# Kernel optimization log

Hardware: AMD Instinct MI355X
Metric: run time of the kernel (lower is better)

Reference implementation:

```python
import jax, jax.numpy as jnp
import numpy as np

EPS = 1e-5
NEG_SLOPE = 0.2


def _minmax(a):
    m = jnp.min(a)
    return (a - m) / (jnp.max(a) - m)


def _bn(x2d, gamma, beta):
    # train-mode BatchNorm1d: stats over axis 0 (biased variance)
    mu = x2d.mean(0)
    var = x2d.var(0)
    return gamma * (x2d - mu) * jax.lax.rsqrt(var + EPS) + beta


def _leaky(a):
    return jnp.where(a >= 0, a, NEG_SLOPE * a)


def setup_inputs() -> dict:
    key = jax.random.key(0)
    ks = jax.random.split(key, 10)
    B, C, N = 256, 1024, 80
    stdv = 1.0 / np.sqrt(C)
    return {
        "x": jax.random.normal(ks[0], (B, C, N), jnp.float32),
        "out1": jax.random.normal(ks[1], (B, N), jnp.float32),
        "adj_param": jax.random.uniform(ks[2], (N, N), jnp.float32),
        "static_weight": jax.random.uniform(ks[3], (C, C), jnp.float32, -stdv, stdv),
        "dynamic_weight": jax.random.uniform(ks[4], (C, C), jnp.float32, -stdv, stdv),
        "conv_global_w": jax.random.normal(ks[5], (C, C), jnp.float32) * 0.02,
        "conv_global_b": jnp.zeros((C,), jnp.float32),
        "conv_co_w": jax.random.normal(ks[6], (N, 2 * C), jnp.float32) * 0.02,
        "conv_co_b": jnp.zeros((N,), jnp.float32),
        "bn_gamma": jnp.ones((C,), jnp.float32),
        "bn_beta": jnp.zeros((C,), jnp.float32),
        "bng_gamma": jnp.ones((C,), jnp.float32),
        "bng_beta": jnp.zeros((C,), jnp.float32),
    }


def reference(x, out1, adj_param, static_weight, dynamic_weight,
              conv_global_w, conv_global_b, conv_co_w, conv_co_b,
              bn_gamma, bn_beta, bng_gamma, bng_beta):
    B, C, N = x.shape

    # ---- static GCN ----
    sadj = _minmax(adj_param)                               # (N,N)
    D = jax.lax.rsqrt(sadj.sum(1))                          # A.sum(1)^-0.5
    adj = D[:, None] * sadj.T * D[None, :]                  # gen_adj, diag matmuls as broadcast
    support = jnp.einsum('bcn,co->bno', x, static_weight)   # (B,N,C)
    h = jnp.einsum('nm,bmo->bno', adj, support)             # (B,N,C)
    h = _bn(h.reshape(-1, C), bn_gamma, bn_beta).reshape(B, N, C)
    out_static = _leaky(h).transpose(0, 2, 1)               # (B,C,N)
    x2 = x + out_static

    # ---- dynamic graph construction ----
    glb = x2.mean(2)                                        # GAP over nodes -> (B,C)
    glb = glb @ conv_global_w.T + conv_global_b             # 1x1 conv
    glb = _leaky(_bn(glb, bng_gamma, bng_beta))             # BN over batch (L=1)
    cat = jnp.concatenate([jnp.broadcast_to(glb[:, :, None], (B, C, N)), x2], axis=1)  # (B,2C,N)
    dadj = jnp.einsum('oc,bcn->bon', conv_co_w, cat) + conv_co_b[None, :, None]        # (B,N,N)
    dadj = _minmax(dadj)

    # ---- adjacency loss ----
    t1 = jnp.einsum('bn,bnm->bm', out1, dadj) / N
    loss = jnp.sum(jnp.linalg.norm(out1 - t1, axis=1))
    loss = loss + jnp.sum(jnp.linalg.norm((dadj - sadj).reshape(B, -1), axis=1))

    # ---- dynamic GCN ----
    Dd = jax.lax.rsqrt(dadj.sum(2))                         # (B,N)
    tadj = Dd[:, :, None] * dadj.transpose(0, 2, 1) * Dd[:, None, :]
    sup = jnp.einsum('bcn,co->bno', x2, dynamic_weight)
    h2 = jnp.einsum('bnm,bmo->bno', tadj, sup)
    h2 = _bn(h2.reshape(-1, C), bn_gamma, bn_beta).reshape(B, N, C).transpose(0, 2, 1)
    h2 = _leaky(h2)                                         # (B,C,N)
    return h2, loss
```

## Files before the change

### kernel.cpp

```cpp
#include <hip/hip_runtime.h>
#include <hip/hip_bf16.h>
#include <math.h>

#define TPB 256

constexpr int   B_  = 256;
constexpr int   C_  = 1024;
constexpr int   N_  = 80;
constexpr int   BNr = B_ * N_;
constexpr int   CN  = C_ * N_;
constexpr long  BCN = (long)B_ * C_ * N_;
constexpr int   NN  = N_ * N_;
constexpr int   BNN = B_ * NN;
constexpr float EPSf = 1e-5f;

typedef __bf16 bf16x8 __attribute__((ext_vector_type(8)));
typedef float  f32x4  __attribute__((ext_vector_type(4)));

__device__ __forceinline__ float leakyf(float v) { return v >= 0.0f ? v : 0.2f * v; }

__device__ __forceinline__ ushort f2bf(float f) {
  __hip_bfloat16 h = __float2bfloat16(f);
  ushort u; __builtin_memcpy(&u, &h, 2); return u;
}
__device__ __forceinline__ float b2f(ushort u) {
  __hip_bfloat16 h; __builtin_memcpy(&h, &u, 2);
  return __bfloat162float(h);
}

#define GLOBAL_AS __attribute__((address_space(1)))
#define LDS_AS    __attribute__((address_space(3)))
__device__ __forceinline__ void load_lds16(const void* g, void* l) {
  __builtin_amdgcn_global_load_lds((const GLOBAL_AS void*)g, (LDS_AS void*)l, 16, 0, 0);
}

__global__ __launch_bounds__(256) void k_prep_all(
    const float* __restrict__ Ws, const float* __restrict__ Wd,
    const float* __restrict__ Wco, const float* __restrict__ Wg,
    ushort* __restrict__ Wts, ushort* __restrict__ Wtd,
    ushort* __restrict__ Wco1t, ushort* __restrict__ Wco2t, ushort* __restrict__ Wg_bf,
    float* __restrict__ zbase,
    const float* __restrict__ ap, float* __restrict__ sadj,
    ushort* __restrict__ adj_bf, float* __restrict__ lossa) {
  __shared__ float sh[NN];
  __shared__ float red[TPB];
  __shared__ float sD[N_];
  __shared__ float s_lo, s_hi;
  const int t = threadIdx.x;
  const int blk = blockIdx.x;
  if (blk < 2048) {
    const float* W = (blk < 1024) ? Ws : Wd;
    ushort* Wt = (blk < 1024) ? Wts : Wtd;
    const int bb = blk & 1023;
    const int bx = bb & 31, by = bb >> 5;
    const int tx = t % 32, ty = t / 32;
    const int r0 = by * 32, c0 = bx * 32;
#pragma unroll
    for (int k = 0; k < 4; ++k) sh[(ty + 8 * k) * 33 + tx] = W[(size_t)(r0 + ty + 8 * k) * C_ + c0 + tx];
    __syncthreads();
#pragma unroll
    for (int k = 0; k < 4; ++k) Wt[(size_t)(c0 + ty + 8 * k) * C_ + r0 + tx] = f2bf(sh[tx * 33 + ty + 8 * k]);
  } else if (blk < 2208) {
    const int i4 = ((blk - 2048) * TPB + t) * 4;
    const int o = i4 >> 11, k = i4 & 2047;
    float4 v = *(const float4*)&Wco[(size_t)o * 2048 + k];
    ushort4 u;
    u.x = f2bf(v.x); u.y = f2bf(v.y); u.z = f2bf(v.z); u.w = f2bf(v.w);
    if (k < C_) *(ushort4*)&Wco1t[(size_t)o * C_ + k] = u;
    else        *(ushort4*)&Wco2t[(size_t)o * C_ + (k - C_)] = u;
  } else if (blk < 3232) {
    const long i4 = ((long)(blk - 2208) * TPB + t) * 4;
    float4 v = *(const float4*)&Wg[i4];
    ushort4 u;
    u.x = f2bf(v.x); u.y = f2bf(v.y); u.z = f2bf(v.z); u.w = f2bf(v.w);
    *(ushort4*)&Wg_bf[i4] = u;
  } else if (blk < 3258) {
    const int i = ((blk - 3232) * TPB + t) * 4;
    float4 z = make_float4(0.f, 0.f, 0.f, 0.f);
    *(float4*)&zbase[i] = z;
  } else {
    float lo = 3.4e38f, hi = -3.4e38f;
    for (int i = t; i < NN; i += TPB) { float v = ap[i]; sh[i] = v; lo = fminf(lo, v); hi = fmaxf(hi, v); }
    red[t] = lo; __syncthreads();
    for (int o = 128; o > 0; o >>= 1) { if (t < o) red[t] = fminf(red[t], red[t + o]); __syncthreads(); }
    if (t == 0) s_lo = red[0];
    __syncthreads();
    red[t] = hi; __syncthreads();
    for (int o = 128; o > 0; o >>= 1) { if (t < o) red[t] = fmaxf(red[t], red[t + o]); __syncthreads(); }
    if (t == 0) s_hi = red[0];
    __syncthreads();
    const float inv = 1.0f / (s_hi - s_lo);
    for (int i = t; i < NN; i += TPB) { float v = (sh[i] - s_lo) * inv; sh[i] = v; sadj[i] = v; }
    __syncthreads();
    if (t < N_) { float sum = 0.f; for (int m = 0; m < N_; ++m) sum += sh[t * N_ + m]; sD[t] = rsqrtf(sum); }
    if (t == 0) *lossa = 0.0f;
    __syncthreads();
    for (int i = t; i < N_ * 96; i += TPB) {
      const int n = i / 96, m = i % 96;
      adj_bf[i] = f2bf((m < N_) ? sD[n] * sh[m * N_ + n] * sD[m] : 0.0f);
    }
  }
}

__global__ __launch_bounds__(256) void k_fold_mfma(const float* __restrict__ Xf32,
                                                   const ushort* __restrict__ Xbf,
                                                   const void* __restrict__ adjsrc,
                                                   ushort* __restrict__ outp, int mode,
                                                   const float* __restrict__ bmin,
                                                   const float* __restrict__ bmax,
                                                   const float* __restrict__ sadj,
                                                   const float* __restrict__ out1,
                                                   float* __restrict__ lossa) {
  __shared__ __align__(16) ushort sX[128][104];
  __shared__ __align__(16) ushort sAdj[80][104];
  __shared__ float sD[N_];
  __shared__ float rl[TPB], rh[TPB];
  __shared__ float s_lo, s_inv;
  const int t = threadIdx.x;
  const int b  = blockIdx.x >> 3;
  const int c0 = (blockIdx.x & 7) * 128;

  if (mode == 0) {
    const ushort* ab = (const ushort*)adjsrc;
    for (int i = t; i < (N_ * 96) / 4; i += TPB) {
      ushort4 v = *(const ushort4*)&ab[i * 4];
      *(ushort4*)&sAdj[(i * 4) / 96][(i * 4) % 96] = v;
    }
    __syncthreads();
  } else {
    rl[t] = (t < 160) ? bmin[t] : 3.4e38f;
    rh[t] = (t < 160) ? bmax[t] : -3.4e38f;
    __syncthreads();
    for (int o = 128; o > 0; o >>= 1) {
      if (t < o) { rl[t] = fminf(rl[t], rl[t + o]); rh[t] = fmaxf(rh[t], rh[t + o]); }
      __syncthreads();
    }
    if (t == 0) { s_lo = rl[0]; s_inv = 1.0f / (rh[0] - rl[0]); }
    __syncthreads();
    const float lo = s_lo, inv = s_inv;
    float* sF = (float*)&sX[0][0];
    const float* db = (const float*)adjsrc + (size_t)b * NN;
    for (int i = t; i < NN / 4; i += TPB) {
      float4 v = *(const float4*)&db[i * 4];
      v.x = (v.x - lo) * inv; v.y = (v.y - lo) * inv;
      v.z = (v.z - lo) * inv; v.w = (v.w - lo) * inv;
      *(float4*)&sF[i * 4] = v;
    }
    __syncthreads();
    if (t < N_) { float s = 0.f; for (int m = 0; m < N_; ++m) s += sF[t * N_ + m]; sD[t] = rsqrtf(s); }
    __syncthreads();
    for (int i = t; i < N_ * 96; i += TPB) {
      const int n = i / 96, m = i % 96;
      sAdj[n][m] = f2bf((m < N_) ? sF[m * N_ + n] * sD[n] * sD[m] : 0.0f);
    }
    __syncthreads();
    if ((blockIdx.x & 7) == 0) {
      const float* o1 = out1 + b * N_;
      float p2 = 0.f;
      for (int i = t; i < NN; i += TPB) { const float d = sF[i] - sadj[i]; p2 += d * d; }
      float p1 = 0.f;
      if (t < N_) {
        float a = 0.f;
        for (int n = 0; n < N_; ++n) a += o1[n] * sF[n * N_ + t];
        const float d = o1[t] - a * (1.0f / N_);
        p1 = d * d;
      }
      rl[t] = p2; rh[t] = p1;
      __syncthreads();
      for (int o = 128; o > 0; o >>= 1) {
        if (t < o) { rl[t] += rl[t + o]; rh[t] += rh[t + o]; }
        __syncthreads();
      }
      if (t == 0) atomicAdd(lossa, sqrtf(rl[0]) + sqrtf(rh[0]));
      __syncthreads();
    }
  }

  if (mode == 0) {
    const float* Xb = Xf32 + ((size_t)b * C_ + c0) * N_;
    for (int i = t; i < (128 * N_) / 4; i += TPB) {
      float4 v = *(const float4*)&Xb[i * 4];
      const int r = (i * 4) / N_, m = (i * 4) % N_;
      ushort4 u; u.x = f2bf(v.x); u.y = f2bf(v.y); u.z = f2bf(v.z); u.w = f2bf(v.w);
      *(ushort4*)&sX[r][m] = u;
    }
  } else {
    const ushort* Xb = Xbf + ((size_t)b * C_ + c0) * N_;
    for (int i = t; i < (128 * N_) / 8; i += TPB) {
      const int r = i / 10, m = (i % 10) * 8;
      uint4 v = *(const uint4*)&Xb[(size_t)r * N_ + m];
      *(uint4*)&sX[r][m] = v;
    }
  }
  for (int i = t; i < (128 * 16) / 4; i += TPB) {
    const int r = i / 4, m = 80 + (i % 4) * 4;
    ushort4 z; z.x = 0; z.y = 0; z.z = 0; z.w = 0;
    *(ushort4*)&sX[r][m] = z;
  }
  __syncthreads();

  const int lane = t & 63, wid = t >> 6;
  const int l16 = lane & 15, lq = lane >> 4;
  f32x4 acc[2][5];
#pragma unroll
  for (int i = 0; i < 2; ++i)
#pragma unroll
    for (int j = 0; j < 5; ++j) { f32x4 z = {0.f, 0.f, 0.f, 0.f}; acc[i][j] = z; }
  bf16x8 af[2][3], bfr[5][3];
#pragma unroll
  for (int i = 0; i < 2; ++i)
#pragma unroll
    for (int kk = 0; kk < 3; ++kk)
      af[i][kk] = *(const bf16x8*)&sX[wid * 32 + i * 16 + l16][kk * 32 + lq * 8];
#pragma unroll
  for (int j = 0; j < 5; ++j)
#pragma unroll
    for (int kk = 0; kk < 3; ++kk)
      bfr[j][kk] = *(const bf16x8*)&sAdj[j * 16 + l16][kk * 32 + lq * 8];
#pragma unroll
  for (int i = 0; i < 2; ++i)
#pragma unroll
    for (int j = 0; j < 5; ++j)
#pragma unroll
      for (int kk = 0; kk < 3; ++kk)
        acc[i][j] = __builtin_amdgcn_mfma_f32_16x16x32_bf16(af[i][kk], bfr[j][kk], acc[i][j], 0, 0, 0);

  ushort* ob = outp + (size_t)b * CN;
#pragma unroll
  for (int i = 0; i < 2; ++i) {
    const int c = c0 + wid * 32 + i * 16 + lq * 4;
#pragma unroll
    for (int j = 0; j < 5; ++j) {
      const int n = j * 16 + l16;
      ushort4 u;
      u.x = f2bf(acc[i][j][0]); u.y = f2bf(acc[i][j][1]);
      u.z = f2bf(acc[i][j][2]); u.w = f2bf(acc[i][j][3]);
      *(ushort4*)&ob[(size_t)n * C_ + c] = u;
    }
  }
}

__global__ __launch_bounds__(256, 2) void k_gemm_160(const ushort* __restrict__ A,
                                                     const ushort* __restrict__ Bt,
                                                     void* __restrict__ outp, int out_bf,
                                                     float* __restrict__ bnsum,
                                                     float* __restrict__ bnsq) {
  __shared__ ushort sA[2][160 * 64];
  __shared__ ushort sB[2][128 * 64];
  const int t = threadIdx.x;
  const int lane = t & 63, wid = t >> 6;
  const int wm = wid >> 1, wn = wid & 1;
  const int l16 = lane & 15, lq = lane >> 4;

  const int lin = blockIdx.x;
  const int xcd = lin & 7, bi = lin >> 3;
  const int tm = xcd * 16 + (bi >> 3);
  const int tn = bi & 7;
  const int m0 = tm * 160, o0 = tn * 128;

  const int srow = t >> 3;
  const int sswz = ((t & 7) ^ ((t >> 3) & 7)) * 8;

  f32x4 acc[5][4];
#pragma unroll
  for (int i = 0; i < 5; ++i)
#pragma unroll
    for (int j = 0; j < 4; ++j) { f32x4 z = {0.f, 0.f, 0.f, 0.f}; acc[i][j] = z; }

#define STA(PAR, ROWB, KT) load_lds16(A  + (size_t)(m0 + (ROWB) + srow) * C_ + (KT) * 64 + sswz, \
                                      &sA[PAR][((ROWB) + (wid << 3)) * 64])
#define STB(PAR, ROWB, KT) load_lds16(Bt + (size_t)(o0 + (ROWB) + srow) * C_ + (KT) * 64 + sswz, \
                                      &sB[PAR][((ROWB) + (wid << 3)) * 64])
#define STAGE_T(PAR, KT) { STA(PAR, 0, KT); STA(PAR, 32, KT); STA(PAR, 64, KT); \
                           STA(PAR, 96, KT); STA(PAR, 128, KT); \
                           STB(PAR, 0, KT); STB(PAR, 32, KT); STB(PAR, 64, KT); STB(PAR, 96, KT); }

#define PH(PAR, KK, STAGES, VMW)                                                          \
  {                                                                                       \
    STAGES                                                                                \
    bf16x8 afr[5], bfr[4];                                                                \
    _Pragma("unroll") for (int fi = 0; fi < 5; ++fi)                                      \
      afr[fi] = *(const bf16x8*)&sA[PAR][(wm * 80 + fi * 16 + l16) * 64 +                 \
                                         (((KK) * 4 + lq) ^ (l16 & 7)) * 8];              \
    _Pragma("unroll") for (int gi = 0; gi < 4; ++gi)                                      \
      bfr[gi] = *(const bf16x8*)&sB[PAR][(wn * 64 + gi * 16 + l16) * 64 +                 \
                                         (((KK) * 4 + lq) ^ (l16 & 7)) * 8];              \
    asm volatile("s_barrier" ::: "memory");                                               \
    asm volatile("s_waitcnt lgkmcnt(0)" ::: "memory");                                    \
    __builtin_amdgcn_s_setprio(1);                                                        \
    _Pragma("unroll") for (int fi = 0; fi < 5; ++fi)                                      \
      _Pragma("unroll") for (int gi = 0; gi < 4; ++gi)                                    \
        acc[fi][gi] = __builtin_amdgcn_mfma_f32_16x16x32_bf16(afr[fi], bfr[gi],           \
                                                              acc[fi][gi], 0, 0, 0);      \
    __builtin_amdgcn_s_setprio(0);                                                        \
    VMW                                                                                   \
    asm volatile("s_barrier" ::: "memory");                                               \
  }

  STAGE_T(0, 0);
  asm volatile("s_waitcnt vmcnt(0)" ::: "memory");
  asm volatile("s_barrier" ::: "memory");

  for (int i = 0; i < 8; ++i) {
    const int t1 = 2 * i + 1, t2 = 2 * i + 2;
    PH(0, 0, { STAGE_T(1, t1); }, {})
    PH(0, 1, {}, { asm volatile("s_waitcnt vmcnt(0)" ::: "memory"); })
    PH(1, 0, { if (i < 7) STAGE_T(0, t2); }, {})
    PH(1, 1, {}, { if (i < 7) { asm volatile("s_waitcnt vmcnt(0)" ::: "memory"); } })
  }

#pragma unroll
  for (int fi = 0; fi < 5; ++fi) {
    const int mg = m0 + wm * 80 + fi * 16 + lq * 4;
    const int b  = mg / 80;
    const int n0 = mg - b * 80;
#pragma unroll
    for (int gi = 0; gi < 4; ++gi) {
      const int og = o0 + wn * 64 + gi * 16 + l16;
      const size_t off = (size_t)b * CN + (size_t)og * N_ + n0;
      if (out_bf) {
        ushort4 u;
        u.x = f2bf(acc[fi][gi][0]); u.y = f2bf(acc[fi][gi][1]);
        u.z = f2bf(acc[fi][gi][2]); u.w = f2bf(acc[fi][gi][3]);
        *(ushort4*)((ushort*)outp + off) = u;
      } else {
        *(f32x4*)((float*)outp + off) = acc[fi][gi];
      }
    }
  }

  {
    float* redS = (float*)&sA[0][0];
    float* redQ = redS + 1024;
    const int slot = wm * 4 + lq;
#pragma unroll
    for (int gi = 0; gi < 4; ++gi) {
      float s = 0.f, q = 0.f;
#pragma unroll
      for (int fi = 0; fi < 5; ++fi)
#pragma unroll
        for (int r = 0; r < 4; ++r) { const float v = acc[fi][gi][r]; s += v; q += v * v; }
      const int ol = wn * 64 + gi * 16 + l16;
      redS[ol * 8 + slot] = s;
      redQ[ol * 8 + slot] = q;
    }
    __syncthreads();
    if (t < 128) {
      float s = 0.f, q = 0.f;
#pragma unroll
      for (int k = 0; k < 8; ++k) { s += redS[t * 8 + k]; q += redQ[t * 8 + k]; }
      atomicAdd(&bnsum[o0 + t], s);
      atomicAdd(&bnsq[o0 + t], q);
    }
  }
#undef STA
#undef STB
#undef STAGE_T
#undef PH
}

__global__ __launch_bounds__(256) void k_dadj_mfma(const ushort* __restrict__ A,
                                                   const ushort* __restrict__ Bw,
                                                   const float* __restrict__ go,
                                                   const float* __restrict__ bco,
                                                   float* __restrict__ dadj,
                                                   float* __restrict__ bmin,
                                                   float* __restrict__ bmax) {
  __shared__ ushort smA[128 * 32];
  __shared__ ushort smB[80 * 32];
  const int t = threadIdx.x;
  const int lane = t & 63, wid = t >> 6;
  const int m0 = blockIdx.x * 128;
  const int rto = t >> 2, ch = t & 3;
  const size_t gA0 = (size_t)(m0 + rto) * C_ + (size_t)ch * 8;
  ushort* ldsA = smA + wid * 512;
  const int l16 = lane & 15, lq = lane >> 4;
  const int wrow = wid * 32;
  f32x4 zero = {0.f, 0.f, 0.f, 0.f};
  f32x4 acc[2][5];
#pragma unroll
  for (int i = 0; i < 2; ++i)
#pragma unroll
    for (int j = 0; j < 5; ++j) acc[i][j] = zero;
  for (int k0 = 0; k0 < C_; k0 += 32) {
    load_lds16(A + gA0 + k0,            ldsA);
    load_lds16(A + gA0 + 64 * C_ + k0,  ldsA + 2048);
    {
      const int idx = t;
      uint4 v = *(const uint4*)&Bw[(size_t)(idx >> 2) * C_ + k0 + (idx & 3) * 8];
      *(uint4*)&smB[idx * 8] = v;
      if (t < 64) {
        const int idx2 = 256 + t;
        uint4 v2 = *(const uint4*)&Bw[(size_t)(idx2 >> 2) * C_ + k0 + (idx2 & 3) * 8];
        *(uint4*)&smB[idx2 * 8] = v2;
      }
    }
    __syncthreads();
    bf16x8 af[2], bfr[5];
#pragma unroll
    for (int i = 0; i < 2; ++i) af[i]  = *(const bf16x8*)&smA[(wrow + i * 16 + l16) * 32 + lq * 8];
#pragma unroll
    for (int j = 0; j < 5; ++j) bfr[j] = *(const bf16x8*)&smB[(j * 16 + l16) * 32 + lq * 8];
#pragma unroll
    for (int i = 0; i < 2; ++i)
#pragma unroll
      for (int j = 0; j < 5; ++j)
        acc[i][j] = __builtin_amdgcn_mfma_f32_16x16x32_bf16(af[i], bfr[j], acc[i][j], 0, 0, 0);
    __syncthreads();
  }
  float vlo = 3.4e38f, vhi = -3.4e38f;
#pragma unroll
  for (int i = 0; i < 2; ++i) {
    const int mg = m0 + wrow + i * 16 + lq * 4;
    const int b  = mg / 80;
    const int n0 = mg - b * 80;
    const float* gob = go + b * N_;
#pragma unroll
    for (int j = 0; j < 5; ++j) {
      const int o = j * 16 + l16;
      const float g = gob[o] + bco[o];
      f32x4 v = acc[i][j];
      v[0] += g; v[1] += g; v[2] += g; v[3] += g;
      vlo = fminf(vlo, fminf(fminf(v[0], v[1]), fminf(v[2], v[3])));
      vhi = fmaxf(vhi, fmaxf(fmaxf(v[0], v[1]), fmaxf(v[2], v[3])));
      *(f32x4*)&dadj[(size_t)b * NN + (size_t)o * N_ + n0] = v;
    }
  }
  float* red = (float*)smA;
  red[t] = vlo; red[TPB + t] = vhi;
  __syncthreads();
  for (int o = 128; o > 0; o >>= 1) {
    if (t < o) {
      red[t] = fminf(red[t], red[t + o]);
      red[TPB + t] = fmaxf(red[TPB + t], red[TPB + t + o]);
    }
    __syncthreads();
  }
  if (t == 0) { bmin[blockIdx.x] = red[0]; bmax[blockIdx.x] = red[TPB]; }
}

__global__ __launch_bounds__(256) void k_glb_mfma(const ushort* __restrict__ A,
                                                  const ushort* __restrict__ Bw,
                                                  const float* __restrict__ bias,
                                                  float* __restrict__ outp,
                                                  float* __restrict__ gsum,
                                                  float* __restrict__ gsq) {
  __shared__ ushort smA[2][64 * 32];
  __shared__ ushort smB[2][64 * 32];
  const int t = threadIdx.x;
  const int lane = t & 63, wid = t >> 6;
  const int o0 = blockIdx.x * 64, m0 = blockIdx.y * 64;
  const int rto = t >> 2, ch = t & 3;
  const size_t gA0 = (size_t)(m0 + rto) * C_ + (size_t)ch * 8;
  const size_t gB0 = (size_t)(o0 + rto) * C_ + (size_t)ch * 8;
  const int l16 = lane & 15, lq = lane >> 4;
  const int wm = wid & 1, wn = wid >> 1;
  f32x4 zero = {0.f, 0.f, 0.f, 0.f};
  f32x4 acc[2][2];
#pragma unroll
  for (int i = 0; i < 2; ++i)
#pragma unroll
    for (int j = 0; j < 2; ++j) acc[i][j] = zero;
  for (int k0 = 0; k0 < C_; k0 += 64) {
    load_lds16(A  + gA0 + k0,       smA[0] + wid * 512);
    load_lds16(A  + gA0 + k0 + 32,  smA[1] + wid * 512);
    load_lds16(Bw + gB0 + k0,       smB[0] + wid * 512);
    load_lds16(Bw + gB0 + k0 + 32,  smB[1] + wid * 512);
    __syncthreads();
#pragma unroll
    for (int h = 0; h < 2; ++h) {
      bf16x8 af[2], bfr[2];
#pragma unroll
      for (int i = 0; i < 2; ++i) af[i]  = *(const bf16x8*)&smA[h][(wm * 32 + i * 16 + l16) * 32 + lq * 8];
#pragma unroll
      for (int j = 0; j < 2; ++j) bfr[j] = *(const bf16x8*)&smB[h][(wn * 32 + j * 16 + l16) * 32 + lq * 8];
#pragma unroll
      for (int i = 0; i < 2; ++i)
#pragma unroll
        for (int j = 0; j < 2; ++j)
          acc[i][j] = __builtin_amdgcn_mfma_f32_16x16x32_bf16(af[i], bfr[j], acc[i][j], 0, 0, 0);
    }
    __syncthreads();
  }
  float ssv[2] = {0.f, 0.f}, sqv[2] = {0.f, 0.f};
#pragma unroll
  for (int i = 0; i < 2; ++i) {
    const int mg = m0 + wm * 32 + i * 16 + lq * 4;
#pragma unroll
    for (int j = 0; j < 2; ++j) {
      const int og = o0 + wn * 32 + j * 16 + l16;
      const float bs = bias[og];
      f32x4 v = acc[i][j];
#pragma unroll
      for (int r = 0; r < 4; ++r) {
        const float val = v[r] + bs;
        outp[(size_t)(mg + r) * C_ + og] = val;
        ssv[j] += val; sqv[j] += val * val;
      }
    }
  }
  {
    float* redS = (float*)&smA[0][0];
    float* redQ = redS + 512;
    const int slot = wm * 4 + lq;
#pragma unroll
    for (int j = 0; j < 2; ++j) {
      const int ol = wn * 32 + j * 16 + l16;
      redS[ol * 8 + slot] = ssv[j];
      redQ[ol * 8 + slot] = sqv[j];
    }
    __syncthreads();
    if (t < 64) {
      float s = 0.f, q = 0.f;
#pragma unroll
      for (int k = 0; k < 8; ++k) { s += redS[t * 8 + k]; q += redQ[t * 8 + k]; }
      atomicAdd(&gsum[o0 + t], s);
      atomicAdd(&gsq[o0 + t], q);
    }
  }
}

__global__ __launch_bounds__(256) void k_go_mfma(const float* __restrict__ glb1,
                                                 const ushort* __restrict__ Bw,
                                                 const float* __restrict__ gsum,
                                                 const float* __restrict__ gsq,
                                                 const float* __restrict__ gg,
                                                 const float* __restrict__ gb,
                                                 float* __restrict__ go) {
  __shared__ ushort smA[128 * 32];
  __shared__ ushort smB[80 * 32];
  __shared__ float pgm[C_], pmu[C_], pgb[C_];
  const int t = threadIdx.x;
  const int lane = t & 63, wid = t >> 6;
  const int kbase = blockIdx.x * 128;
  const int m0 = blockIdx.y * 128;
  const int rto = t >> 2, ch = t & 3;
  const int l16 = lane & 15, lq = lane >> 4;
  const int wrow = wid * 32;
  for (int c = t; c < C_; c += TPB) {
    const float mu = gsum[c] * (1.0f / B_);
    const float var = gsq[c] * (1.0f / B_) - mu * mu;
    pgm[c] = gg[c] * rsqrtf(var + EPSf); pmu[c] = mu; pgb[c] = gb[c];
  }
  __syncthreads();
  f32x4 zero = {0.f, 0.f, 0.f, 0.f};
  f32x4 acc[2][5];
#pragma unroll
  for (int i = 0; i < 2; ++i)
#pragma unroll
    for (int j = 0; j < 5; ++j) acc[i][j] = zero;
  for (int kk0 = 0; kk0 < 128; kk0 += 32) {
    const int k0 = kbase + kk0;
#pragma unroll
    for (int h = 0; h < 2; ++h) {
      const float* src = &glb1[(size_t)(m0 + h * 64 + rto) * C_ + k0 + ch * 8];
      float4 a0 = *(const float4*)src;
      float4 a1 = *(const float4*)(src + 4);
      float av[8] = {a0.x, a0.y, a0.z, a0.w, a1.x, a1.y, a1.z, a1.w};
      ushort4 u0, u1;
      const int cb = k0 + ch * 8;
      u0.x = f2bf(leakyf(pgm[cb+0]*(av[0]-pmu[cb+0])+pgb[cb+0]));
      u0.y = f2bf(leakyf(pgm[cb+1]*(av[1]-pmu[cb+1])+pgb[cb+1]));
      u0.z = f2bf(leakyf(pgm[cb+2]*(av[2]-pmu[cb+2])+pgb[cb+2]));
      u0.w = f2bf(leakyf(pgm[cb+3]*(av[3]-pmu[cb+3])+pgb[cb+3]));
      u1.x = f2bf(leakyf(pgm[cb+4]*(av[4]-pmu[cb+4])+pgb[cb+4]));
      u1.y = f2bf(leakyf(pgm[cb+5]*(av[5]-pmu[cb+5])+pgb[cb+5]));
      u1.z = f2bf(leakyf(pgm[cb+6]*(av[6]-pmu[cb+6])+pgb[cb+6]));
      u1.w = f2bf(leakyf(pgm[cb+7]*(av[7]-pmu[cb+7])+pgb[cb+7]));
      *(ushort4*)&smA[h * 2048 + t * 8]     = u0;
      *(ushort4*)&smA[h * 2048 + t * 8 + 4] = u1;
    }
    {
      const int idx = t;
      uint4 v = *(const uint4*)&Bw[(size_t)(idx >> 2) * C_ + k0 + (idx & 3) * 8];
      *(uint4*)&smB[idx * 8] = v;
      if (t < 64) {
        const int idx2 = 256 + t;
        uint4 v2 = *(const uint4*)&Bw[(size_t)(idx2 >> 2) * C_ + k0 + (idx2 & 3) * 8];
        *(uint4*)&smB[idx2 * 8] = v2;
      }
    }
    __syncthreads();
    bf16x8 af[2], bfr[5];
#pragma unroll
    for (int i = 0; i < 2; ++i) af[i]  = *(const bf16x8*)&smA[(wrow + i * 16 + l16) * 32 + lq * 8];
#pragma unroll
    for (int j = 0; j < 5; ++j) bfr[j] = *(const bf16x8*)&smB[(j * 16 + l16) * 32 + lq * 8];
#pragma unroll
    for (int i = 0; i < 2; ++i)
#pragma unroll
      for (int j = 0; j < 5; ++j)
        acc[i][j] = __builtin_amdgcn_mfma_f32_16x16x32_bf16(af[i], bfr[j], acc[i][j], 0, 0, 0);
    __syncthreads();
  }
#pragma unroll
  for (int i = 0; i < 2; ++i) {
    const int mg = m0 + wrow + i * 16 + lq * 4;
#pragma unroll
    for (int j = 0; j < 5; ++j) {
      const int o = j * 16 + l16;
#pragma unroll
      for (int r = 0; r < 4; ++r)
        atomicAdd(&go[(size_t)(mg + r) * N_ + o], acc[i][j][r]);
    }
  }
}

__global__ __launch_bounds__(256) void k_x2_fused(
    const float* __restrict__ x, ushort* __restrict__ hx,
    const float* __restrict__ g, const float* __restrict__ be,
    const float* __restrict__ ssum, const float* __restrict__ ssq,
    ushort* __restrict__ x2t, ushort* __restrict__ glb0b) {
  __shared__ float s[64][85];
  __shared__ float pg[64], pm[64], pb[64];
  const int t = threadIdx.x;
  const long row0 = (long)blockIdx.x * 64;
  const int b = (int)(row0 >> 10), c0 = (int)(row0 & 1023);
  if (t < 64) {
    const int c = c0 + t;
    const float mu = ssum[c] * (1.0f / BNr);
    const float var = ssq[c] * (1.0f / BNr) - mu * mu;
    const float rstd = rsqrtf(var + EPSf);
    pg[t] = g[c] * rstd; pm[t] = mu; pb[t] = be[c];
  }
  __syncthreads();
  const float* xb = x  + row0 * N_;
  ushort*      hb = hx + row0 * N_;
  for (int i4 = t; i4 < (64 * N_) / 4; i4 += TPB) {
    const int e = i4 * 4, r = e / N_, n = e % N_;
    float4 xv = *(const float4*)&xb[e];
    ushort4 hu = *(const ushort4*)&hb[e];
    const float gm = pg[r], m = pm[r], bb = pb[r];
    float4 o;
    o.x = xv.x + leakyf(gm * (b2f(hu.x) - m) + bb);
    o.y = xv.y + leakyf(gm * (b2f(hu.y) - m) + bb);
    o.z = xv.z + leakyf(gm * (b2f(hu.z) - m) + bb);
    o.w = xv.w + leakyf(gm * (b2f(hu.w) - m) + bb);
    *(float4*)&s[r][n] = o;
    ushort4 ou;
    ou.x = f2bf(o.x); ou.y = f2bf(o.y); ou.z = f2bf(o.z); ou.w = f2bf(o.w);
    *(ushort4*)&hb[e] = ou;
  }
  __syncthreads();
  const int tx = t % 16, ty = t / 16;
  ushort* tb = x2t + (size_t)b * CN + c0 + tx * 4;
#pragma unroll
  for (int u = 0; u < 5; ++u) {
    const int n = ty + 16 * u;
    ushort4 v;
    v.x = f2bf(s[tx * 4 + 0][n]); v.y = f2bf(s[tx * 4 + 1][n]);
    v.z = f2bf(s[tx * 4 + 2][n]); v.w = f2bf(s[tx * 4 + 3][n]);
    *(ushort4*)&tb[(size_t)n * C_] = v;
  }
  {
    const int r = t >> 2, q = t & 3;
    float sacc = 0.f;
    for (int n = q; n < N_; n += 4) sacc += s[r][n];
    sacc += __shfl_down(sacc, 1);
    sacc += __shfl_down(sacc, 2);
    if (q == 0) glb0b[(size_t)b * C_ + c0 + r] = f2bf(sacc * (1.0f / N_));
  }
}

__global__ void k_final(const ushort* __restrict__ h2, float* __restrict__ outp,
                        const float* __restrict__ g, const float* __restrict__ be,
                        const float* __restrict__ ssum, const float* __restrict__ ssq,
                        const float* __restrict__ lossa) {
  const long i = ((long)blockIdx.x * TPB + threadIdx.x) * 4;
  const int c = (int)((i / N_) % C_);
  ushort4 hu = *(const ushort4*)&h2[i];
  const float mu = ssum[c] * (1.0f / BNr);
  const float rstd = rsqrtf(ssq[c] * (1.0f / BNr) - mu * mu + EPSf);
  const float gm = g[c] * rstd, bb = be[c];
  float4 v;
  v.x = leakyf(gm * (b2f(hu.x) - mu) + bb);
  v.y = leakyf(gm * (b2f(hu.y) - mu) + bb);
  v.z = leakyf(gm * (b2f(hu.z) - mu) + bb);
  v.w = leakyf(gm * (b2f(hu.w) - mu) + bb);
  *(float4*)&outp[i] = v;
  if (blockIdx.x == 0 && threadIdx.x == 0) outp[BCN] = *lossa;
}

extern "C" void kernel_launch(void* const* d_in, const int* in_sizes, int n_in,
                              void* d_out, int out_size, void* d_ws, size_t ws_size,
                              hipStream_t stream) {
  const float* x    = (const float*)d_in[0];
  const float* out1 = (const float*)d_in[1];
  const float* ap   = (const float*)d_in[2];
  const float* Ws   = (const float*)d_in[3];
  const float* Wd   = (const float*)d_in[4];
  const float* Wg   = (const float*)d_in[5];
  const float* bg   = (const float*)d_in[6];
  const float* Wco  = (const float*)d_in[7];
  const float* bco  = (const float*)d_in[8];
  const float* bn_g  = (const float*)d_in[9];
  const float* bn_b  = (const float*)d_in[10];
  const float* bng_g = (const float*)d_in[11];
  const float* bng_b = (const float*)d_in[12];
  float* out = (float*)d_out;

  float* w = (float*)d_ws;
  float* sadj  = w;
  float* dadj  = sadj + NN;
  float* glb0  = dadj + BNN;
  float* glb1  = glb0 + B_ * C_;
  float* go    = glb1 + B_ * C_;
  float* ssum1 = go + BNr;
  float* ssq1  = ssum1 + C_;
  float* ssum2 = ssq1 + C_;
  float* ssq2  = ssum2 + C_;
  float* gsum  = ssq2 + C_;
  float* gsq   = gsum + C_;
  float* bmin  = gsq + C_;
  float* bmax  = bmin + 512;
  float* lossa = bmax + 512;
  ushort* ub   = (ushort*)(((uintptr_t)(lossa + 1) + 255) & ~(uintptr_t)255);
  ushort* xa_bf  = ub;
  ushort* hT_bf  = xa_bf + BCN;
  ushort* Wts    = hT_bf + BCN;
  ushort* Wtd    = Wts + (size_t)C_ * C_;
  ushort* Wco2t  = Wtd + (size_t)C_ * C_;
  ushort* adj_bf = Wco2t + (size_t)N_ * C_;
  ushort* Wg_bf   = (ushort*)dadj;
  ushort* Wco1t   = (ushort*)dadj + (size_t)C_ * C_;
  ushort* glb0_bf = (ushort*)glb0;
  ushort* x2t_bf  = xa_bf;

  k_prep_all<<<3259, TPB, 0, stream>>>(Ws, Wd, Wco, Wg, Wts, Wtd, Wco1t, Wco2t, Wg_bf,
                                       go, ap, sadj, adj_bf, lossa);

  k_fold_mfma<<<B_ * 8, TPB, 0, stream>>>(x, hT_bf, adj_bf, xa_bf, 0, bmin, bmax,
                                          sadj, out1, lossa);
  k_gemm_160<<<1024, TPB, 0, stream>>>(xa_bf, Wts, hT_bf, 1, ssum1, ssq1);
  k_x2_fused<<<(B_ * C_) / 64, TPB, 0, stream>>>(x, hT_bf, bn_g, bn_b, ssum1, ssq1,
                                                 x2t_bf, glb0_bf);

  k_glb_mfma<<<dim3(C_ / 64, B_ / 64), TPB, 0, stream>>>(glb0_bf, Wg_bf, bg, glb1, gsum, gsq);
  k_go_mfma<<<dim3(8, B_ / 128), TPB, 0, stream>>>(glb1, Wco1t, gsum, gsq, bng_g, bng_b, go);
  k_dadj_mfma<<<BNr / 128, TPB, 0, stream>>>(x2t_bf, Wco2t, go, bco, dadj, bmin, bmax);

  k_fold_mfma<<<B_ * 8, TPB, 0, stream>>>(x, hT_bf, dadj, xa_bf, 1, bmin, bmax,
                                          sadj, out1, lossa);
  k_gemm_160<<<1024, TPB, 0, stream>>>(xa_bf, Wtd, hT_bf, 1, ssum2, ssq2);
  k_final<<<(int)(BCN / (4 * TPB)), TPB, 0, stream>>>(hT_bf, out, bn_g, bn_b, ssum2, ssq2, lossa);
}
```

Before: 467.2 us.

## Build dynamic normalized adjacency once per batch in a separate kernel

The per-batch normalized dynamic adjacency and loss terms move out of the fold kernel into a new k_tadj kernel that runs one block per batch. Before, each of the 8 blocks per batch recomputed the same min/max reduction, degree normalization and bf16 transpose. The fold kernel now reads the precomputed bf16 adjacency and the X rows straight from global memory into MFMA fragments, skipping LDS staging and barriers. In exchange it adds a kernel launch and a global round trip for the adjacency. Fragments are read from global without LDS reuse, which may cost more memory traffic.

Measured after the change: 443.9 us. 5.0% less time.

```diff
diff --git a/kernel.cpp b/kernel.cpp
--- a/kernel.cpp
+++ b/kernel.cpp
@@ -12,6 +12,7 @@
 constexpr long  BCN = (long)B_ * C_ * N_;
 constexpr int   NN  = N_ * N_;
 constexpr int   BNN = B_ * NN;
+constexpr int   ADJP = N_ * 96;
 constexpr float EPSf = 1e-5f;
 
 typedef __bf16 bf16x8 __attribute__((ext_vector_type(8)));
@@ -95,135 +96,118 @@
     if (t < N_) { float sum = 0.f; for (int m = 0; m < N_; ++m) sum += sh[t * N_ + m]; sD[t] = rsqrtf(sum); }
     if (t == 0) *lossa = 0.0f;
     __syncthreads();
-    for (int i = t; i < N_ * 96; i += TPB) {
+    for (int i = t; i < ADJP; i += TPB) {
       const int n = i / 96, m = i % 96;
       adj_bf[i] = f2bf((m < N_) ? sD[n] * sh[m * N_ + n] * sD[m] : 0.0f);
     }
   }
 }
 
-__global__ __launch_bounds__(256) void k_fold_mfma(const float* __restrict__ Xf32,
-                                                   const ushort* __restrict__ Xbf,
-                                                   const void* __restrict__ adjsrc,
-                                                   ushort* __restrict__ outp, int mode,
-                                                   const float* __restrict__ bmin,
-                                                   const float* __restrict__ bmax,
-                                                   const float* __restrict__ sadj,
-                                                   const float* __restrict__ out1,
-                                                   float* __restrict__ lossa) {
-  __shared__ __align__(16) ushort sX[128][104];
-  __shared__ __align__(16) ushort sAdj[80][104];
+__global__ __launch_bounds__(256) void k_tadj(const float* __restrict__ dadj,
+                                              const float* __restrict__ bmin,
+                                              const float* __restrict__ bmax,
+                                              const float* __restrict__ sadj,
+                                              const float* __restrict__ out1,
+                                              ushort* __restrict__ tadj,
+                                              float* __restrict__ lossa) {
+  __shared__ float sF[NN];
   __shared__ float sD[N_];
   __shared__ float rl[TPB], rh[TPB];
   __shared__ float s_lo, s_inv;
   const int t = threadIdx.x;
+  const int b = blockIdx.x;
+  rl[t] = (t < 160) ? bmin[t] : 3.4e38f;
+  rh[t] = (t < 160) ? bmax[t] : -3.4e38f;
+  __syncthreads();
+  for (int o = 128; o > 0; o >>= 1) {
+    if (t < o) { rl[t] = fminf(rl[t], rl[t + o]); rh[t] = fmaxf(rh[t], rh[t + o]); }
+    __syncthreads();
+  }
+  if (t == 0) { s_lo = rl[0]; s_inv = 1.0f / (rh[0] - rl[0]); }
+  __syncthreads();
+  const float lo = s_lo, inv = s_inv;
+  const float* db = dadj + (size_t)b * NN;
+  for (int i = t; i < NN / 4; i += TPB) {
+    float4 v = *(const float4*)&db[i * 4];
+    v.x = (v.x - lo) * inv; v.y = (v.y - lo) * inv;
+    v.z = (v.z - lo) * inv; v.w = (v.w - lo) * inv;
+    *(float4*)&sF[i * 4] = v;
+  }
+  __syncthreads();
+  if (t < N_) { float s = 0.f; for (int m = 0; m < N_; ++m) s += sF[t * N_ + m]; sD[t] = rsqrtf(s); }
+  __syncthreads();
+  ushort* tb = tadj + (size_t)b * ADJP;
+  for (int i = t; i < ADJP; i += TPB) {
+    const int n = i / 96, m = i % 96;
+    tb[i] = f2bf((m < N_) ? sF[m * N_ + n] * sD[n] * sD[m] : 0.0f);
+  }
+  const float* o1 = out1 + b * N_;
+  float p2 = 0.f;
+  for (int i = t; i < NN; i += TPB) { const float d = sF[i] - sadj[i]; p2 += d * d; }
+  float p1 = 0.f;
+  if (t < N_) {
+    float a = 0.f;
+    for (int n = 0; n < N_; ++n) a += o1[n] * sF[n * N_ + t];
+    const float d = o1[t] - a * (1.0f / N_);
+    p1 = d * d;
+  }
+  rl[t] = p2; rh[t] = p1;
+  __syncthreads();
+  for (int o = 128; o > 0; o >>= 1) {
+    if (t < o) { rl[t] += rl[t + o]; rh[t] += rh[t + o]; }
+    __syncthreads();
+  }
+  if (t == 0) atomicAdd(lossa, sqrtf(rl[0]) + sqrtf(rh[0]));
+}
+
+__global__ __launch_bounds__(256) void k_fold(const float* __restrict__ Xf32,
+                                              const ushort* __restrict__ Xbf,
+                                              const ushort* __restrict__ adjb,
+                                              ushort* __restrict__ outp, int mode) {
+  const int t = threadIdx.x;
   const int b  = blockIdx.x >> 3;
   const int c0 = (blockIdx.x & 7) * 128;
-
-  if (mode == 0) {
-    const ushort* ab = (const ushort*)adjsrc;
-    for (int i = t; i < (N_ * 96) / 4; i += TPB) {
-      ushort4 v = *(const ushort4*)&ab[i * 4];
-      *(ushort4*)&sAdj[(i * 4) / 96][(i * 4) % 96] = v;
-    }
-    __syncthreads();
-  } else {
-    rl[t] = (t < 160) ? bmin[t] : 3.4e38f;
-    rh[t] = (t < 160) ? bmax[t] : -3.4e38f;
-    __syncthreads();
-    for (int o = 128; o > 0; o >>= 1) {
-      if (t < o) { rl[t] = fminf(rl[t], rl[t + o]); rh[t] = fmaxf(rh[t], rh[t + o]); }
-      __syncthreads();
-    }
-    if (t == 0) { s_lo = rl[0]; s_inv = 1.0f / (rh[0] - rl[0]); }
-    __syncthreads();
-    const float lo = s_lo, inv = s_inv;
-    float* sF = (float*)&sX[0][0];
-    const float* db = (const float*)adjsrc + (size_t)b * NN;
-    for (int i = t; i < NN / 4; i += TPB) {
-      float4 v = *(const float4*)&db[i * 4];
-      v.x = (v.x - lo) * inv; v.y = (v.y - lo) * inv;
-      v.z = (v.z - lo) * inv; v.w = (v.w - lo) * inv;
-      *(float4*)&sF[i * 4] = v;
-    }
-    __syncthreads();
-    if (t < N_) { float s = 0.f; for (int m = 0; m < N_; ++m) s += sF[t * N_ + m]; sD[t] = rsqrtf(s); }
-    __syncthreads();
-    for (int i = t; i < N_ * 96; i += TPB) {
-      const int n = i / 96, m = i % 96;
-      sAdj[n][m] = f2bf((m < N_) ? sF[m * N_ + n] * sD[n] * sD[m] : 0.0f);
-    }
-    __syncthreads();
-    if ((blockIdx.x & 7) == 0) {
-      const float* o1 = out1 + b * N_;
-      float p2 = 0.f;
-      for (int i = t; i < NN; i += TPB) { const float d = sF[i] - sadj[i]; p2 += d * d; }
-      float p1 = 0.f;
-      if (t < N_) {
-        float a = 0.f;
-        for (int n = 0; n < N_; ++n) a += o1[n] * sF[n * N_ + t];
-        const float d = o1[t] - a * (1.0f / N_);
-        p1 = d * d;
-      }
-      rl[t] = p2; rh[t] = p1;
-      __syncthreads();
-      for (int o = 128; o > 0; o >>= 1) {
-        if (t < o) { rl[t] += rl[t + o]; rh[t] += rh[t + o]; }
-        __syncthreads();
-      }
-      if (t == 0) atomicAdd(lossa, sqrtf(rl[0]) + sqrtf(rh[0]));
-      __syncthreads();
-    }
-  }
-
-  if (mode == 0) {
-    const float* Xb = Xf32 + ((size_t)b * C_ + c0) * N_;
-    for (int i = t; i < (128 * N_) / 4; i += TPB) {
-      float4 v = *(const float4*)&Xb[i * 4];
-      const int r = (i * 4) / N_, m = (i * 4) % N_;
-      ushort4 u; u.x = f2bf(v.x); u.y = f2bf(v.y); u.z = f2bf(v.z); u.w = f2bf(v.w);
-      *(ushort4*)&sX[r][m] = u;
-    }
-  } else {
-    const ushort* Xb = Xbf + ((size_t)b * C_ + c0) * N_;
-    for (int i = t; i < (128 * N_) / 8; i += TPB) {
-      const int r = i / 10, m = (i % 10) * 8;
-      uint4 v = *(const uint4*)&Xb[(size_t)r * N_ + m];
-      *(uint4*)&sX[r][m] = v;
-    }
-  }
-  for (int i = t; i < (128 * 16) / 4; i += TPB) {
-    const int r = i / 4, m = 80 + (i % 4) * 4;
-    ushort4 z; z.x = 0; z.y = 0; z.z = 0; z.w = 0;
-    *(ushort4*)&sX[r][m] = z;
-  }
-  __syncthreads();
-
   const int lane = t & 63, wid = t >> 6;
   const int l16 = lane & 15, lq = lane >> 4;
+  const ushort* ab = adjb + (mode ? (size_t)b * ADJP : 0);
+
   f32x4 acc[2][5];
 #pragma unroll
   for (int i = 0; i < 2; ++i)
 #pragma unroll
     for (int j = 0; j < 5; ++j) { f32x4 z = {0.f, 0.f, 0.f, 0.f}; acc[i][j] = z; }
-  bf16x8 af[2][3], bfr[5][3];
-#pragma unroll
-  for (int i = 0; i < 2; ++i)
-#pragma unroll
-    for (int kk = 0; kk < 3; ++kk)
-      af[i][kk] = *(const bf16x8*)&sX[wid * 32 + i * 16 + l16][kk * 32 + lq * 8];
-#pragma unroll
-  for (int j = 0; j < 5; ++j)
-#pragma unroll
-    for (int kk = 0; kk < 3; ++kk)
-      bfr[j][kk] = *(const bf16x8*)&sAdj[j * 16 + l16][kk * 32 + lq * 8];
-#pragma unroll
-  for (int i = 0; i < 2; ++i)
+
+#pragma unroll
+  for (int kk = 0; kk < 3; ++kk) {
+    const int mf = kk * 32 + lq * 8;
+    bf16x8 b5[5], a2[2];
 #pragma unroll
     for (int j = 0; j < 5; ++j)
-#pragma unroll
-      for (int kk = 0; kk < 3; ++kk)
-        acc[i][j] = __builtin_amdgcn_mfma_f32_16x16x32_bf16(af[i][kk], bfr[j][kk], acc[i][j], 0, 0, 0);
+      b5[j] = *(const bf16x8*)&ab[(j * 16 + l16) * 96 + mf];
+#pragma unroll
+    for (int i = 0; i < 2; ++i) {
+      const int row = wid * 32 + i * 16 + l16;
+      if (mf >= N_) {
+        union { bf16x8 v; uint4 u; } z; z.u = make_uint4(0, 0, 0, 0);
+        a2[i] = z.v;
+      } else if (mode == 0) {
+        const float* src = Xf32 + ((size_t)b * C_ + c0 + row) * N_ + mf;
+        float4 v0 = *(const float4*)src;
+        float4 v1 = *(const float4*)(src + 4);
+        union { bf16x8 v; ushort u[8]; } tmp;
+        tmp.u[0] = f2bf(v0.x); tmp.u[1] = f2bf(v0.y); tmp.u[2] = f2bf(v0.z); tmp.u[3] = f2bf(v0.w);
+        tmp.u[4] = f2bf(v1.x); tmp.u[5] = f2bf(v1.y); tmp.u[6] = f2bf(v1.z); tmp.u[7] = f2bf(v1.w);
+        a2[i] = tmp.v;
+      } else {
+        a2[i] = *(const bf16x8*)&Xbf[((size_t)b * C_ + c0 + row) * N_ + mf];
+      }
+    }
+#pragma unroll
+    for (int i = 0; i < 2; ++i)
+#pragma unroll
+      for (int j = 0; j < 5; ++j)
+        acc[i][j] = __builtin_amdgcn_mfma_f32_16x16x32_bf16(a2[i], b5[j], acc[i][j], 0, 0, 0);
+  }
 
   ushort* ob = outp + (size_t)b * CN;
 #pragma unroll
@@ -721,6 +705,7 @@
   ushort* Wtd    = Wts + (size_t)C_ * C_;
   ushort* Wco2t  = Wtd + (size_t)C_ * C_;
   ushort* adj_bf = Wco2t + (size_t)N_ * C_;
+  ushort* tadj_bf = adj_bf + ADJP;
   ushort* Wg_bf   = (ushort*)dadj;
   ushort* Wco1t   = (ushort*)dadj + (size_t)C_ * C_;
   ushort* glb0_bf = (ushort*)glb0;
@@ -729,8 +714,7 @@
   k_prep_all<<<3259, TPB, 0, stream>>>(Ws, Wd, Wco, Wg, Wts, Wtd, Wco1t, Wco2t, Wg_bf,
                                        go, ap, sadj, adj_bf, lossa);
 
-  k_fold_mfma<<<B_ * 8, TPB, 0, stream>>>(x, hT_bf, adj_bf, xa_bf, 0, bmin, bmax,
-                                          sadj, out1, lossa);
+  k_fold<<<B_ * 8, TPB, 0, stream>>>(x, hT_bf, adj_bf, xa_bf, 0);
   k_gemm_160<<<1024, TPB, 0, stream>>>(xa_bf, Wts, hT_bf, 1, ssum1, ssq1);
   k_x2_fused<<<(B_ * C_) / 64, TPB, 0, stream>>>(x, hT_bf, bn_g, bn_b, ssum1, ssq1,
                                                  x2t_bf, glb0_bf);
@@ -739,8 +723,9 @@
   k_go_mfma<<<dim3(8, B_ / 128), TPB, 0, stream>>>(glb1, Wco1t, gsum, gsq, bng_g, bng_b, go);
   k_dadj_mfma<<<BNr / 128, TPB, 0, stream>>>(x2t_bf, Wco2t, go, bco, dadj, bmin, bmax);
 
-  k_fold_mfma<<<B_ * 8, TPB, 0, stream>>>(x, hT_bf, dadj, xa_bf, 1, bmin, bmax,
-                                          sadj, out1, lossa);
+  k_tadj<<<B_, TPB, 0, stream>>>(dadj, bmin, bmax, sadj, out1, tadj_bf, lossa);
+
+  k_fold<<<B_ * 8, TPB, 0, stream>>>(x, hT_bf, tadj_bf, xa_bf, 1);
   k_gemm_160<<<1024, TPB, 0, stream>>>(xa_bf, Wtd, hT_bf, 1, ssum2, ssq2);
   k_final<<<(int)(BCN / (4 * TPB)), TPB, 0, stream>>>(hT_bf, out, bn_g, bn_b, ssum2, ssq2, lossa);
 }
```
